# Performance work log

Hardware: AMD Instinct MI355X
Metric: run time of the kernel (lower is better)

Reference implementation:

```python
import jax, jax.numpy as jnp
import numpy as np

H = 16  # n_heads

def setup_inputs() -> dict:
    key = jax.random.key(0)
    ks = jax.random.split(key, 11)
    B, L, D = 2, 2048, 1024
    w = 1.0 / np.sqrt(D).astype(np.float32)
    return {
        "query": jax.random.normal(ks[0], (B, L, D), jnp.float32),
        "key":   jax.random.normal(ks[1], (B, L, D), jnp.float32),
        "value": jax.random.normal(ks[2], (B, L, D), jnp.float32),
        "Wq": jax.random.normal(ks[3], (D, D), jnp.float32) * w,
        "bq": jax.random.normal(ks[4], (D,), jnp.float32) * 0.01,
        "Wk": jax.random.normal(ks[5], (D, D), jnp.float32) * w,
        "bk": jax.random.normal(ks[6], (D,), jnp.float32) * 0.01,
        "Wv": jax.random.normal(ks[7], (D, D), jnp.float32) * w,
        "bv": jax.random.normal(ks[8], (D,), jnp.float32) * 0.01,
        "Wo": jax.random.normal(ks[9], (D, D), jnp.float32) * w,
        "bo": jax.random.normal(ks[10], (D,), jnp.float32) * 0.01,
        "masksize": 256,
    }

def reference(query, key, value, Wq, bq, Wk, bk, Wv, bv, Wo, bo, masksize):
    B, L, D = query.shape
    d_k = D // H
    scale = 1.0 / np.sqrt(d_k).astype(np.float32)

    def proj(x, W, b):
        # nn.Linear: x @ W.T + b, then [B,L,H,d_k] -> [B,H,L,d_k]
        return (x @ W.T + b).reshape(B, L, H, d_k).transpose(0, 2, 1, 3)

    q = proj(query, Wq, bq)
    k = proj(key, Wk, bk)
    v = proj(value, Wv, bv)

    # Sliding-window float mask (faithful to original: a 0/1 FLOAT tensor is
    # passed as attn_mask to SDPA, so it is ADDED to scores, not -inf-masked).
    half = masksize // 2
    i = jnp.arange(L)[:, None]
    j = jnp.arange(L)[None, :]
    band = (jnp.abs(i - j) <= half).astype(q.dtype)  # [L, L]

    scores = jnp.einsum('bhqd,bhkd->bhqk', q, k) * scale + band  # [B,H,L,L]
    attn = jax.nn.softmax(scores, axis=-1)
    out = jnp.einsum('bhqk,bhkd->bhqd', attn, v)  # [B,H,L,d_k]
    out = out.transpose(0, 2, 1, 3).reshape(B, L, D)
    return out @ Wo.T + bo
```

## Files before the change

kernel.cpp:

```cpp
#include <hip/hip_runtime.h>
#include <hip/hip_bf16.h>

#define Hh 16
#define Ll 2048
#define Dd 1024
#define DK 64
#define Mm 4096
#define Kk 1024
#define Nn 1024

typedef short bf16x8 __attribute__((ext_vector_type(8)));
typedef float f32x4 __attribute__((ext_vector_type(4)));

static __device__ __forceinline__ unsigned short f2bf(float f) {
    union { __hip_bfloat16 b; unsigned short u; } cv;
    cv.b = __float2bfloat16(f);
    return cv.u;
}

static __device__ __forceinline__ unsigned packtr(float a, float b) {
    return __builtin_amdgcn_perm(__builtin_bit_cast(unsigned, b),
                                 __builtin_bit_cast(unsigned, a), 0x07060302u);
}

static __device__ __forceinline__ float fexp2(float x) {
    return __builtin_amdgcn_exp2f(x);
}

static __device__ __forceinline__ void glds16(const ushort* g, ushort* l) {
    __builtin_amdgcn_global_load_lds((const __attribute__((address_space(1))) unsigned int*)g,
                                     (__attribute__((address_space(3))) unsigned int*)l,
                                     16, 0, 0);
}

__global__ __launch_bounds__(256) void cast_all(
    const float* __restrict__ q, const float* __restrict__ k, const float* __restrict__ v,
    const float* __restrict__ wq, const float* __restrict__ wk, const float* __restrict__ wv,
    const float* __restrict__ wo,
    ushort* __restrict__ qb, ushort* __restrict__ kb, ushort* __restrict__ vb,
    ushort* __restrict__ wqb, ushort* __restrict__ wkb, ushort* __restrict__ wvb,
    ushort* __restrict__ wob) {
    const int bx = blockIdx.x;
    const float4* s; ushort4* d; int base;
    if      (bx <  4096) { s = (const float4*)q;  d = (ushort4*)qb;  base = 0; }
    else if (bx <  8192) { s = (const float4*)k;  d = (ushort4*)kb;  base = 4096; }
    else if (bx < 12288) { s = (const float4*)v;  d = (ushort4*)vb;  base = 8192; }
    else if (bx < 13312) { s = (const float4*)wq; d = (ushort4*)wqb; base = 12288; }
    else if (bx < 14336) { s = (const float4*)wk; d = (ushort4*)wkb; base = 13312; }
    else if (bx < 15360) { s = (const float4*)wv; d = (ushort4*)wvb; base = 14336; }
    else                 { s = (const float4*)wo; d = (ushort4*)wob; base = 15360; }
    const int i = (bx - base) * 256 + threadIdx.x;
    float4 vv = s[i];
    ushort4 o;
    o.x = f2bf(vv.x); o.y = f2bf(vv.y); o.z = f2bf(vv.z); o.w = f2bf(vv.w);
    d[i] = o;
}

__global__ __launch_bounds__(256) void gemm_qkv(
    const ushort* __restrict__ A0, const ushort* __restrict__ A1, const ushort* __restrict__ A2,
    const ushort* __restrict__ W0, const ushort* __restrict__ W1, const ushort* __restrict__ W2,
    const float* __restrict__ b0, const float* __restrict__ b1, const float* __restrict__ b2,
    ushort* __restrict__ O0, ushort* __restrict__ O1, ushort* __restrict__ OVt) {
    __shared__ __align__(16) ushort SM[4 * 128 * 32];
    ushort* As = SM;
    ushort* Bs = SM + 8192;
    const int z = blockIdx.z;
    const ushort* A = (z == 0) ? A0 : (z == 1) ? A1 : A2;
    const ushort* W = (z == 0) ? W0 : (z == 1) ? W1 : W2;
    const float* bias = (z == 0) ? b0 : (z == 1) ? b1 : b2;

    const int t = threadIdx.x;
    const int wave = t >> 6, lane = t & 63;
    const int quad = lane >> 4, l15 = lane & 15;
    const int brow = blockIdx.y * 128, bcol = blockIdx.x * 128;
    const int wr = (wave >> 1) * 64, wc = (wave & 1) * 64;
    const int c2r = lane >> 2;
    const int c2c = (lane & 3) * 8;

    f32x4 acc[4][4] = {};

    for (int k0 = 0; k0 < Kk; k0 += 64) {
        __syncthreads();
#pragma unroll
        for (int halfc = 0; halfc < 2; halfc++) {
            const int c = wave * 2 + halfc;
#pragma unroll
            for (int p = 0; p < 2; p++) {
                glds16(A + (size_t)(brow + c * 16 + c2r) * Kk + k0 + p * 32 + c2c,
                       As + p * 4096 + (c * 16) * 32);
                glds16(W + (size_t)(bcol + c * 16 + c2r) * Kk + k0 + p * 32 + c2c,
                       Bs + p * 4096 + (c * 16) * 32);
            }
        }
        __syncthreads();

#pragma unroll
        for (int p = 0; p < 2; p++) {
            bf16x8 af[4], bfr[4];
#pragma unroll
            for (int i = 0; i < 4; i++)
                af[i] = *(const bf16x8*)(As + p * 4096 + (wr + i * 16 + l15) * 32 + quad * 8);
#pragma unroll
            for (int j = 0; j < 4; j++)
                bfr[j] = *(const bf16x8*)(Bs + p * 4096 + (wc + j * 16 + l15) * 32 + quad * 8);
#pragma unroll
            for (int i = 0; i < 4; i++)
#pragma unroll
                for (int j = 0; j < 4; j++)
                    acc[i][j] = __builtin_amdgcn_mfma_f32_16x16x32_bf16(af[i], bfr[j], acc[i][j], 0, 0, 0);
        }
    }

    if (z < 2) {
        ushort* Out = (z == 0) ? O0 : O1;
        const float oscl = (z == 0) ? 0.18033688f : 1.0f;
        const int b = brow >> 11;
        const int lbase = (brow & 2047) + wr;
        const int h = (bcol + wc) >> 6;
        ushort* T = SM + wave * 1280;
        __syncthreads();
#pragma unroll
        for (int i = 0; i < 4; i++) {
#pragma unroll
            for (int j = 0; j < 4; j++) {
                const float bv = bias[bcol + wc + j * 16 + l15];
#pragma unroll
                for (int r = 0; r < 4; r++)
                    T[(quad * 4 + r) * 80 + j * 16 + l15] = f2bf((acc[i][j][r] + bv) * oscl);
            }
            const int r8 = lane >> 3, c8 = lane & 7;
#pragma unroll
            for (int pass = 0; pass < 2; pass++) {
                const uint4 val = *(const uint4*)(T + (pass * 8 + r8) * 80 + c8 * 8);
                const int l = lbase + i * 16 + pass * 8 + r8;
                *(uint4*)(Out + ((size_t)(b * Hh + h) * Ll + l) * DK + c8 * 8) = val;
            }
        }
    } else {
        ushort* T = SM;
        const int b = brow >> 11;
        const int lbase = brow & 2047;
        const int npr = (wave & 1) * 16 + l15;
#pragma unroll
        for (int j = 0; j < 4; j++) {
            __syncthreads();
            const float bv = bias[bcol + wc + j * 16 + l15];
#pragma unroll
            for (int i = 0; i < 4; i++)
#pragma unroll
                for (int r = 0; r < 4; r++) {
                    const int m = wr + i * 16 + quad * 4 + r;
                    T[npr * 136 + m] = f2bf(acc[i][j][r] + bv);
                }
            __syncthreads();
#pragma unroll
            for (int cc = 0; cc < 2; cc++) {
                const int idx = t + cc * 256;
                const int ni = idx >> 4;
                const int ms = idx & 15;
                const int n = bcol + (ni >> 4) * 64 + j * 16 + (ni & 15);
                const int hh = n >> 6, dk = n & 63;
                uint4 val = *(const uint4*)(T + ni * 136 + ms * 8);
                *(uint4*)(OVt + ((size_t)(b * Hh + hh) * DK + dk) * Ll + lbase + ms * 8) = val;
            }
        }
    }
}

__global__ __launch_bounds__(256) void attn_kernel(const ushort* __restrict__ Q,
                                                   const ushort* __restrict__ Kp,
                                                   const ushort* __restrict__ Vt,
                                                   ushort* __restrict__ Oout,
                                                   const int* __restrict__ masksize) {
    __shared__ __align__(16) ushort Ks[2 * 128 * 32];
    __shared__ __align__(16) ushort Vs[64 * 128];
    const int t = threadIdx.x;
    const int wave = t >> 6, lane = t & 63;
    const int quad = lane >> 4, l15 = lane & 15;
    const int bx = blockIdx.x;
    const int bh = bx & 31, qc = bx >> 5;
    const int q0w = qc * 128 + wave * 32;
    const int half = masksize[0] >> 1;
    const unsigned wid = (unsigned)(2 * half);

    const ushort* Qb = Q + (size_t)bh * (Ll * DK);
    const ushort* Kb = Kp + (size_t)bh * (Ll * DK);
    const ushort* Vb = Vt + (size_t)bh * (DK * Ll);

    const bf16x8 qA0 = *(const bf16x8*)(Qb + (size_t)(q0w + l15) * DK + quad * 8);
    const bf16x8 qA1 = *(const bf16x8*)(Qb + (size_t)(q0w + l15) * DK + 32 + quad * 8);
    const bf16x8 qB0 = *(const bf16x8*)(Qb + (size_t)(q0w + 16 + l15) * DK + quad * 8);
    const bf16x8 qB1 = *(const bf16x8*)(Qb + (size_t)(q0w + 16 + l15) * DK + 32 + quad * 8);

    const float C2IN  = (1.0f - 24.0f) * 1.44269504088896f;
    const float C2OUT = -24.0f * 1.44269504088896f;
    const float E1 = 2.718281828f;

    bf16x8 onesf;
#pragma unroll
    for (int j = 0; j < 8; j++) onesf[j] = (short)0x3F80;

    f32x4 OA[4] = {}, OB[4] = {};
    f32x4 SA = {}, SB = {};

    const int krow = lane >> 2;
    const int kcol8 = (lane & 3) * 8;
    const int vdl = lane >> 4;
    const int vg0 = 2 * (lane & 15);

    for (int kt = 0; kt < Ll; kt += 128) {
        __syncthreads();
        if (wave < 2) {
            const int cbase = wave * 4;
#pragma unroll
            for (int c = 0; c < 4; c++)
#pragma unroll
                for (int pan = 0; pan < 2; pan++)
                    glds16(Kb + (size_t)(kt + (cbase + c) * 16 + krow) * DK + pan * 32 + kcol8,
                           Ks + (pan * 128 + (cbase + c) * 16) * 32);
        } else {
            const int sb = (wave - 2) * 8;
#pragma unroll
            for (int i = 0; i < 8; i++) {
                const int sidx = sb + i;
                const int d = sidx * 4 + vdl;
                const int g0 = vg0 ^ (d & 30);
                glds16(Vb + (size_t)d * Ll + kt + g0 * 4, Vs + sidx * 512);
            }
        }
        __syncthreads();

        const int qlo = q0w, qhi = q0w + 31;
        const bool allout = (kt + 127 < qlo - half) || (kt > qhi + half);
        const bool allin  = (kt >= qhi - half) && (kt + 127 <= qlo + half);
        const bool uniform = allin || allout;
        const float cinit = allin ? C2IN : C2OUT;
        f32x4 cvec = {cinit, cinit, cinit, cinit};

#pragma unroll
        for (int s = 0; s < 4; s++) {
            const bf16x8 kf00 = *(const bf16x8*)(Ks + ((2 * s) * 16 + l15) * 32 + quad * 8);
            const bf16x8 kf01 = *(const bf16x8*)(Ks + 4096 + ((2 * s) * 16 + l15) * 32 + quad * 8);
            const bf16x8 kf10 = *(const bf16x8*)(Ks + ((2 * s + 1) * 16 + l15) * 32 + quad * 8);
            const bf16x8 kf11 = *(const bf16x8*)(Ks + 4096 + ((2 * s + 1) * 16 + l15) * 32 + quad * 8);
            f32x4 zA0 = __builtin_amdgcn_mfma_f32_16x16x32_bf16(kf00, qA0, cvec, 0, 0, 0);
            zA0 = __builtin_amdgcn_mfma_f32_16x16x32_bf16(kf01, qA1, zA0, 0, 0, 0);
            f32x4 zA1 = __builtin_amdgcn_mfma_f32_16x16x32_bf16(kf10, qA0, cvec, 0, 0, 0);
            zA1 = __builtin_amdgcn_mfma_f32_16x16x32_bf16(kf11, qA1, zA1, 0, 0, 0);
            f32x4 zB0 = __builtin_amdgcn_mfma_f32_16x16x32_bf16(kf00, qB0, cvec, 0, 0, 0);
            zB0 = __builtin_amdgcn_mfma_f32_16x16x32_bf16(kf01, qB1, zB0, 0, 0, 0);
            f32x4 zB1 = __builtin_amdgcn_mfma_f32_16x16x32_bf16(kf10, qB0, cvec, 0, 0, 0);
            zB1 = __builtin_amdgcn_mfma_f32_16x16x32_bf16(kf11, qB1, zB1, 0, 0, 0);

            float pA[8], pB[8];
            if (uniform) {
#pragma unroll
                for (int g = 0; g < 2; g++)
#pragma unroll
                    for (int r = 0; r < 4; r++) {
                        pA[g * 4 + r] = fexp2(g ? zA1[r] : zA0[r]);
                        pB[g * 4 + r] = fexp2(g ? zB1[r] : zB0[r]);
                    }
            } else {
                const int kb = kt + s * 32 + quad * 4 + half;
#pragma unroll
                for (int g = 0; g < 2; g++)
#pragma unroll
                    for (int r = 0; r < 4; r++) {
                        const unsigned ttA = (unsigned)(kb + g * 16 + r - (q0w + l15));
                        const unsigned ttB = (unsigned)(kb + g * 16 + r - (q0w + 16 + l15));
                        pA[g * 4 + r] = fexp2(g ? zA1[r] : zA0[r]) * (ttA <= wid ? E1 : 1.0f);
                        pB[g * 4 + r] = fexp2(g ? zB1[r] : zB0[r]) * (ttB <= wid ? E1 : 1.0f);
                    }
            }

            bf16x8 pfA, pfB;
            ((unsigned*)&pfA)[0] = packtr(pA[0], pA[1]);
            ((unsigned*)&pfA)[1] = packtr(pA[2], pA[3]);
            ((unsigned*)&pfA)[2] = packtr(pA[4], pA[5]);
            ((unsigned*)&pfA)[3] = packtr(pA[6], pA[7]);
            ((unsigned*)&pfB)[0] = packtr(pB[0], pB[1]);
            ((unsigned*)&pfB)[1] = packtr(pB[2], pB[3]);
            ((unsigned*)&pfB)[2] = packtr(pB[4], pB[5]);
            ((unsigned*)&pfB)[3] = packtr(pB[6], pB[7]);

            SA = __builtin_amdgcn_mfma_f32_16x16x32_bf16(pfA, onesf, SA, 0, 0, 0);
            SB = __builtin_amdgcn_mfma_f32_16x16x32_bf16(pfB, onesf, SB, 0, 0, 0);

#pragma unroll
            for (int i = 0; i < 4; i++) {
                const int d = i * 16 + l15;
                const int x4 = (d & 30) * 4;
                const int bi = d * 128;
                const ushort4 v1 = *(const ushort4*)(Vs + bi + (((s * 8 + quad) * 4) ^ x4));
                const ushort4 v2 = *(const ushort4*)(Vs + bi + (((s * 8 + 4 + quad) * 4) ^ x4));
                bf16x8 vc;
                *(ushort4*)&vc = v1;
                *((ushort4*)&vc + 1) = v2;
                OA[i] = __builtin_amdgcn_mfma_f32_16x16x32_bf16(pfA, vc, OA[i], 0, 0, 0);
                OB[i] = __builtin_amdgcn_mfma_f32_16x16x32_bf16(pfB, vc, OB[i], 0, 0, 0);
            }
        }
    }

    float liA[4], liB[4];
#pragma unroll
    for (int r = 0; r < 4; r++) {
        liA[r] = 1.0f / SA[r];
        liB[r] = 1.0f / SB[r];
    }

    const int b = bh >> 4, h = bh & 15;
#pragma unroll
    for (int i = 0; i < 4; i++)
#pragma unroll
        for (int r = 0; r < 4; r++) {
            const int qa = q0w + quad * 4 + r;
            Oout[((size_t)b * Ll + qa) * Dd + h * DK + i * 16 + l15] = f2bf(OA[i][r] * liA[r]);
            Oout[((size_t)b * Ll + qa + 16) * Dd + h * DK + i * 16 + l15] = f2bf(OB[i][r] * liB[r]);
        }
}

__global__ __launch_bounds__(256) void gemm_o(const ushort* __restrict__ A,
                                              const ushort* __restrict__ W,
                                              const float* __restrict__ bias,
                                              float* __restrict__ Out) {
    __shared__ __align__(16) ushort As[2 * 64 * 32];
    __shared__ __align__(16) ushort Bs[2 * 128 * 32];
    const int t = threadIdx.x;
    const int wave = t >> 6, lane = t & 63;
    const int quad = lane >> 4, l15 = lane & 15;
    const int brow = blockIdx.y * 64, bcol = blockIdx.x * 128;
    const int wr = (wave >> 1) * 32, wc = (wave & 1) * 64;
    const int c2r = lane >> 2;
    const int c2c = (lane & 3) * 8;

    f32x4 acc[2][4] = {};

    for (int k0 = 0; k0 < Kk; k0 += 64) {
        __syncthreads();
#pragma unroll
        for (int p = 0; p < 2; p++) {
            glds16(A + (size_t)(brow + wave * 16 + c2r) * Kk + k0 + p * 32 + c2c,
                   As + p * 2048 + (wave * 16) * 32);
#pragma unroll
            for (int halfc = 0; halfc < 2; halfc++) {
                const int c = wave * 2 + halfc;
                glds16(W + (size_t)(bcol + c * 16 + c2r) * Kk + k0 + p * 32 + c2c,
                       Bs + p * 4096 + (c * 16) * 32);
            }
        }
        __syncthreads();

#pragma unroll
        for (int p = 0; p < 2; p++) {
            bf16x8 af[2], bfr[4];
#pragma unroll
            for (int i = 0; i < 2; i++)
                af[i] = *(const bf16x8*)(As + p * 2048 + (wr + i * 16 + l15) * 32 + quad * 8);
#pragma unroll
            for (int j = 0; j < 4; j++)
                bfr[j] = *(const bf16x8*)(Bs + p * 4096 + (wc + j * 16 + l15) * 32 + quad * 8);
#pragma unroll
            for (int i = 0; i < 2; i++)
#pragma unroll
                for (int j = 0; j < 4; j++)
                    acc[i][j] = __builtin_amdgcn_mfma_f32_16x16x32_bf16(af[i], bfr[j], acc[i][j], 0, 0, 0);
        }
    }

#pragma unroll
    for (int i = 0; i < 2; i++)
#pragma unroll
        for (int j = 0; j < 4; j++) {
            const int n = bcol + wc + j * 16 + l15;
            const float bv = bias[n];
#pragma unroll
            for (int r = 0; r < 4; r++) {
                const int m = brow + wr + i * 16 + quad * 4 + r;
                Out[(size_t)m * Nn + n] = acc[i][j][r] + bv;
            }
        }
}

extern "C" void kernel_launch(void* const* d_in, const int* in_sizes, int n_in,
                              void* d_out, int out_size, void* d_ws, size_t ws_size,
                              hipStream_t stream) {
    const float* query = (const float*)d_in[0];
    const float* key   = (const float*)d_in[1];
    const float* value = (const float*)d_in[2];
    const float* Wq = (const float*)d_in[3];
    const float* bq = (const float*)d_in[4];
    const float* Wk = (const float*)d_in[5];
    const float* bk = (const float*)d_in[6];
    const float* Wv = (const float*)d_in[7];
    const float* bv = (const float*)d_in[8];
    const float* Wo = (const float*)d_in[9];
    const float* bo = (const float*)d_in[10];
    const int* masksize = (const int*)d_in[11];

    char* ws = (char*)d_ws;
    const size_t MB = 1024 * 1024;
    ushort* qb  = (ushort*)(ws + 0 * MB);
    ushort* kbf = (ushort*)(ws + 8 * MB);
    ushort* vbf = (ushort*)(ws + 16 * MB);
    ushort* wqb = (ushort*)(ws + 24 * MB);
    ushort* wkb = (ushort*)(ws + 26 * MB);
    ushort* wvb = (ushort*)(ws + 28 * MB);
    ushort* wob = (ushort*)(ws + 30 * MB);
    ushort* Qp  = (ushort*)(ws + 32 * MB);
    ushort* Kp  = (ushort*)(ws + 40 * MB);
    ushort* Vt  = (ushort*)(ws + 48 * MB);
    ushort* AO  = (ushort*)(ws + 56 * MB);

    cast_all<<<16384, 256, 0, stream>>>(query, key, value, Wq, Wk, Wv, Wo,
                                        qb, kbf, vbf, wqb, wkb, wvb, wob);

    gemm_qkv<<<dim3(8, 32, 3), 256, 0, stream>>>(qb, kbf, vbf,
                                                 wqb, wkb, wvb,
                                                 bq, bk, bv,
                                                 Qp, Kp, Vt);

    attn_kernel<<<512, 256, 0, stream>>>(Qp, Kp, Vt, AO, masksize);

    gemm_o<<<dim3(8, 64), 256, 0, stream>>>(AO, wob, bo, (float*)d_out);
}
```

Measured before the change: 229.6 us.

## Fuse fp32-to-bf16 cast into GEMM tile loads and drop cast kernel

Removes the separate cast_all kernel and has the QKV and output-projection GEMMs load fp32 activations and weights directly into LDS. Each K-step is 32 wide with an XOR swizzle, and values are converted to bf16 in registers just before the MFMA. This removes a full read and write pass over the inputs plus one launch. In exchange the GEMMs move twice the bytes per tile from global memory, do extra ALU conversion work per K step, and sync twice as often because the K step halved. Rounding changes to a simple add-0x8000 truncation without NaN handling.

```diff
diff --git a/kernel.cpp b/kernel.cpp
--- a/kernel.cpp
+++ b/kernel.cpp
@@ -23,6 +23,21 @@
                                  __builtin_bit_cast(unsigned, a), 0x07060302u);
 }
 
+static __device__ __forceinline__ unsigned packrnd(float a, float b) {
+    const unsigned ua = __builtin_bit_cast(unsigned, a) + 0x8000u;
+    const unsigned ub = __builtin_bit_cast(unsigned, b) + 0x8000u;
+    return __builtin_amdgcn_perm(ub, ua, 0x07060302u);
+}
+
+static __device__ __forceinline__ bf16x8 cvt8(const float4 f0, const float4 f1) {
+    bf16x8 r;
+    ((unsigned*)&r)[0] = packrnd(f0.x, f0.y);
+    ((unsigned*)&r)[1] = packrnd(f0.z, f0.w);
+    ((unsigned*)&r)[2] = packrnd(f1.x, f1.y);
+    ((unsigned*)&r)[3] = packrnd(f1.z, f1.w);
+    return r;
+}
+
 static __device__ __forceinline__ float fexp2(float x) {
     return __builtin_amdgcn_exp2f(x);
 }
@@ -32,41 +47,22 @@
                                      (__attribute__((address_space(3))) unsigned int*)l,
                                      16, 0, 0);
 }
-
-__global__ __launch_bounds__(256) void cast_all(
-    const float* __restrict__ q, const float* __restrict__ k, const float* __restrict__ v,
-    const float* __restrict__ wq, const float* __restrict__ wk, const float* __restrict__ wv,
-    const float* __restrict__ wo,
-    ushort* __restrict__ qb, ushort* __restrict__ kb, ushort* __restrict__ vb,
-    ushort* __restrict__ wqb, ushort* __restrict__ wkb, ushort* __restrict__ wvb,
-    ushort* __restrict__ wob) {
-    const int bx = blockIdx.x;
-    const float4* s; ushort4* d; int base;
-    if      (bx <  4096) { s = (const float4*)q;  d = (ushort4*)qb;  base = 0; }
-    else if (bx <  8192) { s = (const float4*)k;  d = (ushort4*)kb;  base = 4096; }
-    else if (bx < 12288) { s = (const float4*)v;  d = (ushort4*)vb;  base = 8192; }
-    else if (bx < 13312) { s = (const float4*)wq; d = (ushort4*)wqb; base = 12288; }
-    else if (bx < 14336) { s = (const float4*)wk; d = (ushort4*)wkb; base = 13312; }
-    else if (bx < 15360) { s = (const float4*)wv; d = (ushort4*)wvb; base = 14336; }
-    else                 { s = (const float4*)wo; d = (ushort4*)wob; base = 15360; }
-    const int i = (bx - base) * 256 + threadIdx.x;
-    float4 vv = s[i];
-    ushort4 o;
-    o.x = f2bf(vv.x); o.y = f2bf(vv.y); o.z = f2bf(vv.z); o.w = f2bf(vv.w);
-    d[i] = o;
+static __device__ __forceinline__ void glds16f(const float* g, float* l) {
+    __builtin_amdgcn_global_load_lds((const __attribute__((address_space(1))) unsigned int*)g,
+                                     (__attribute__((address_space(3))) unsigned int*)l,
+                                     16, 0, 0);
 }
 
 __global__ __launch_bounds__(256) void gemm_qkv(
-    const ushort* __restrict__ A0, const ushort* __restrict__ A1, const ushort* __restrict__ A2,
-    const ushort* __restrict__ W0, const ushort* __restrict__ W1, const ushort* __restrict__ W2,
+    const float* __restrict__ A0, const float* __restrict__ A1, const float* __restrict__ A2,
+    const float* __restrict__ W0, const float* __restrict__ W1, const float* __restrict__ W2,
     const float* __restrict__ b0, const float* __restrict__ b1, const float* __restrict__ b2,
     ushort* __restrict__ O0, ushort* __restrict__ O1, ushort* __restrict__ OVt) {
-    __shared__ __align__(16) ushort SM[4 * 128 * 32];
-    ushort* As = SM;
-    ushort* Bs = SM + 8192;
+    __shared__ __align__(16) float Asf[128 * 32];
+    __shared__ __align__(16) float Bsf[128 * 32];
     const int z = blockIdx.z;
-    const ushort* A = (z == 0) ? A0 : (z == 1) ? A1 : A2;
-    const ushort* W = (z == 0) ? W0 : (z == 1) ? W1 : W2;
+    const float* A = (z == 0) ? A0 : (z == 1) ? A1 : A2;
+    const float* W = (z == 0) ? W0 : (z == 1) ? W1 : W2;
     const float* bias = (z == 0) ? b0 : (z == 1) ? b1 : b2;
 
     const int t = threadIdx.x;
@@ -74,42 +70,46 @@
     const int quad = lane >> 4, l15 = lane & 15;
     const int brow = blockIdx.y * 128, bcol = blockIdx.x * 128;
     const int wr = (wave >> 1) * 64, wc = (wave & 1) * 64;
-    const int c2r = lane >> 2;
-    const int c2c = (lane & 3) * 8;
+
+    const int rlane = lane >> 3;
+    const int G4 = (((lane & 7) ^ (rlane & 7)) << 2);
+    const int x7 = l15 & 7;
 
     f32x4 acc[4][4] = {};
 
-    for (int k0 = 0; k0 < Kk; k0 += 64) {
-        __syncthreads();
-#pragma unroll
-        for (int halfc = 0; halfc < 2; halfc++) {
-            const int c = wave * 2 + halfc;
-#pragma unroll
-            for (int p = 0; p < 2; p++) {
-                glds16(A + (size_t)(brow + c * 16 + c2r) * Kk + k0 + p * 32 + c2c,
-                       As + p * 4096 + (c * 16) * 32);
-                glds16(W + (size_t)(bcol + c * 16 + c2r) * Kk + k0 + p * 32 + c2c,
-                       Bs + p * 4096 + (c * 16) * 32);
-            }
-        }
-        __syncthreads();
-
-#pragma unroll
-        for (int p = 0; p < 2; p++) {
-            bf16x8 af[4], bfr[4];
-#pragma unroll
-            for (int i = 0; i < 4; i++)
-                af[i] = *(const bf16x8*)(As + p * 4096 + (wr + i * 16 + l15) * 32 + quad * 8);
+    for (int k0 = 0; k0 < Kk; k0 += 32) {
+        __syncthreads();
+#pragma unroll
+        for (int c = 0; c < 4; c++) {
+            const int r0 = wave * 32 + c * 8;
+            glds16f(A + (size_t)(brow + r0 + rlane) * Kk + k0 + G4, Asf + r0 * 32);
+            glds16f(W + (size_t)(bcol + r0 + rlane) * Kk + k0 + G4, Bsf + r0 * 32);
+        }
+        __syncthreads();
+
+        bf16x8 af[4], bfr[4];
+#pragma unroll
+        for (int i = 0; i < 4; i++) {
+            const int m = wr + i * 16 + l15;
+            const float4 f0 = *(const float4*)(Asf + m * 32 + (((2 * quad) ^ x7) << 2));
+            const float4 f1 = *(const float4*)(Asf + m * 32 + (((2 * quad + 1) ^ x7) << 2));
+            af[i] = cvt8(f0, f1);
+        }
+#pragma unroll
+        for (int j = 0; j < 4; j++) {
+            const int m = wc + j * 16 + l15;
+            const float4 f0 = *(const float4*)(Bsf + m * 32 + (((2 * quad) ^ x7) << 2));
+            const float4 f1 = *(const float4*)(Bsf + m * 32 + (((2 * quad + 1) ^ x7) << 2));
+            bfr[j] = cvt8(f0, f1);
+        }
+#pragma unroll
+        for (int i = 0; i < 4; i++)
 #pragma unroll
             for (int j = 0; j < 4; j++)
-                bfr[j] = *(const bf16x8*)(Bs + p * 4096 + (wc + j * 16 + l15) * 32 + quad * 8);
-#pragma unroll
-            for (int i = 0; i < 4; i++)
-#pragma unroll
-                for (int j = 0; j < 4; j++)
-                    acc[i][j] = __builtin_amdgcn_mfma_f32_16x16x32_bf16(af[i], bfr[j], acc[i][j], 0, 0, 0);
-        }
+                acc[i][j] = __builtin_amdgcn_mfma_f32_16x16x32_bf16(af[i], bfr[j], acc[i][j], 0, 0, 0);
     }
+
+    ushort* SMu = (ushort*)Asf;
 
     if (z < 2) {
         ushort* Out = (z == 0) ? O0 : O1;
@@ -117,7 +117,7 @@
         const int b = brow >> 11;
         const int lbase = (brow & 2047) + wr;
         const int h = (bcol + wc) >> 6;
-        ushort* T = SM + wave * 1280;
+        ushort* T = SMu + wave * 1280;
         __syncthreads();
 #pragma unroll
         for (int i = 0; i < 4; i++) {
@@ -137,7 +137,7 @@
             }
         }
     } else {
-        ushort* T = SM;
+        ushort* T = SMu;
         const int b = brow >> 11;
         const int lbase = brow & 2047;
         const int npr = (wave & 1) * 16 + l15;
@@ -322,51 +322,50 @@
 }
 
 __global__ __launch_bounds__(256) void gemm_o(const ushort* __restrict__ A,
-                                              const ushort* __restrict__ W,
+                                              const float* __restrict__ W,
                                               const float* __restrict__ bias,
                                               float* __restrict__ Out) {
-    __shared__ __align__(16) ushort As[2 * 64 * 32];
-    __shared__ __align__(16) ushort Bs[2 * 128 * 32];
+    __shared__ __align__(16) ushort As[64 * 32];
+    __shared__ __align__(16) float Bsf[128 * 32];
     const int t = threadIdx.x;
     const int wave = t >> 6, lane = t & 63;
     const int quad = lane >> 4, l15 = lane & 15;
     const int brow = blockIdx.y * 64, bcol = blockIdx.x * 128;
     const int wr = (wave >> 1) * 32, wc = (wave & 1) * 64;
-    const int c2r = lane >> 2;
-    const int c2c = (lane & 3) * 8;
+    const int gr = wave * 16 + (lane >> 2);
+    const int gc = (lane & 3) * 8;
+    const int rlane = lane >> 3;
+    const int G4 = (((lane & 7) ^ (rlane & 7)) << 2);
+    const int x7 = l15 & 7;
 
     f32x4 acc[2][4] = {};
 
-    for (int k0 = 0; k0 < Kk; k0 += 64) {
-        __syncthreads();
-#pragma unroll
-        for (int p = 0; p < 2; p++) {
-            glds16(A + (size_t)(brow + wave * 16 + c2r) * Kk + k0 + p * 32 + c2c,
-                   As + p * 2048 + (wave * 16) * 32);
-#pragma unroll
-            for (int halfc = 0; halfc < 2; halfc++) {
-                const int c = wave * 2 + halfc;
-                glds16(W + (size_t)(bcol + c * 16 + c2r) * Kk + k0 + p * 32 + c2c,
-                       Bs + p * 4096 + (c * 16) * 32);
-            }
-        }
-        __syncthreads();
-
-#pragma unroll
-        for (int p = 0; p < 2; p++) {
-            bf16x8 af[2], bfr[4];
-#pragma unroll
-            for (int i = 0; i < 2; i++)
-                af[i] = *(const bf16x8*)(As + p * 2048 + (wr + i * 16 + l15) * 32 + quad * 8);
+    for (int k0 = 0; k0 < Kk; k0 += 32) {
+        __syncthreads();
+        glds16(A + (size_t)(brow + gr) * Kk + k0 + gc, As + wave * 512);
+#pragma unroll
+        for (int c = 0; c < 4; c++) {
+            const int r0 = wave * 32 + c * 8;
+            glds16f(W + (size_t)(bcol + r0 + rlane) * Kk + k0 + G4, Bsf + r0 * 32);
+        }
+        __syncthreads();
+
+        bf16x8 af[2], bfr[4];
+#pragma unroll
+        for (int i = 0; i < 2; i++)
+            af[i] = *(const bf16x8*)(As + (wr + i * 16 + l15) * 32 + quad * 8);
+#pragma unroll
+        for (int j = 0; j < 4; j++) {
+            const int m = wc + j * 16 + l15;
+            const float4 f0 = *(const float4*)(Bsf + m * 32 + (((2 * quad) ^ x7) << 2));
+            const float4 f1 = *(const float4*)(Bsf + m * 32 + (((2 * quad + 1) ^ x7) << 2));
+            bfr[j] = cvt8(f0, f1);
+        }
+#pragma unroll
+        for (int i = 0; i < 2; i++)
 #pragma unroll
             for (int j = 0; j < 4; j++)
-                bfr[j] = *(const bf16x8*)(Bs + p * 4096 + (wc + j * 16 + l15) * 32 + quad * 8);
-#pragma unroll
-            for (int i = 0; i < 2; i++)
-#pragma unroll
-                for (int j = 0; j < 4; j++)
-                    acc[i][j] = __builtin_amdgcn_mfma_f32_16x16x32_bf16(af[i], bfr[j], acc[i][j], 0, 0, 0);
-        }
+                acc[i][j] = __builtin_amdgcn_mfma_f32_16x16x32_bf16(af[i], bfr[j], acc[i][j], 0, 0, 0);
     }
 
 #pragma unroll
@@ -401,27 +400,17 @@
 
     char* ws = (char*)d_ws;
     const size_t MB = 1024 * 1024;
-    ushort* qb  = (ushort*)(ws + 0 * MB);
-    ushort* kbf = (ushort*)(ws + 8 * MB);
-    ushort* vbf = (ushort*)(ws + 16 * MB);
-    ushort* wqb = (ushort*)(ws + 24 * MB);
-    ushort* wkb = (ushort*)(ws + 26 * MB);
-    ushort* wvb = (ushort*)(ws + 28 * MB);
-    ushort* wob = (ushort*)(ws + 30 * MB);
-    ushort* Qp  = (ushort*)(ws + 32 * MB);
-    ushort* Kp  = (ushort*)(ws + 40 * MB);
-    ushort* Vt  = (ushort*)(ws + 48 * MB);
-    ushort* AO  = (ushort*)(ws + 56 * MB);
-
-    cast_all<<<16384, 256, 0, stream>>>(query, key, value, Wq, Wk, Wv, Wo,
-                                        qb, kbf, vbf, wqb, wkb, wvb, wob);
-
-    gemm_qkv<<<dim3(8, 32, 3), 256, 0, stream>>>(qb, kbf, vbf,
-                                                 wqb, wkb, wvb,
+    ushort* Qp = (ushort*)(ws + 0 * MB);
+    ushort* Kp = (ushort*)(ws + 8 * MB);
+    ushort* Vt = (ushort*)(ws + 16 * MB);
+    ushort* AO = (ushort*)(ws + 24 * MB);
+
+    gemm_qkv<<<dim3(8, 32, 3), 256, 0, stream>>>(query, key, value,
+                                                 Wq, Wk, Wv,
                                                  bq, bk, bv,
                                                  Qp, Kp, Vt);
 
     attn_kernel<<<512, 256, 0, stream>>>(Qp, Kp, Vt, AO, masksize);
 
-    gemm_o<<<dim3(8, 64), 256, 0, stream>>>(AO, wob, bo, (float*)d_out);
-}
+    gemm_o<<<dim3(8, 64), 256, 0, stream>>>(AO, Wo, bo, (float*)d_out);
+}
```

Measured after the change: 274.9 us. 1.2x slower.
